# Performance work log

Measured on AMD Instinct MI355X. Metric: run time of the kernel, lower is better.

The kernel has to match this reference:

```python
import jax, jax.numpy as jnp
import numpy as np

B, SQ, SKV, D = 8, 2048, 2048, 1024

def setup_inputs() -> dict:
    key = jax.random.key(0)
    ks = jax.random.split(key, 8)
    s = 1.0 / np.sqrt(D)  # torch Linear default init range
    return {
        "target": jax.random.normal(ks[0], (B, SQ, D), dtype=jnp.float32),
        "non_target": jax.random.normal(ks[1], (B, SKV, D), dtype=jnp.float32),
        "Wq": jax.random.uniform(ks[2], (D, D), jnp.float32, -s, s),
        "bq": jax.random.uniform(ks[3], (D,), jnp.float32, -s, s),
        "Wk": jax.random.uniform(ks[4], (D, D), jnp.float32, -s, s),
        "bk": jax.random.uniform(ks[5], (D,), jnp.float32, -s, s),
        "Wv": jax.random.uniform(ks[6], (D, D), jnp.float32, -s, s),
        "bv": jax.random.uniform(ks[7], (D,), jnp.float32, -s, s),
    }

def reference(target, non_target, Wq, bq, Wk, bk, Wv, bv):
    # Linear projections (torch Linear: x @ W.T + b)
    q = jnp.einsum('bsd,ed->bse', target, Wq) + bq       # [B,SQ,D]
    k = jnp.einsum('bsd,ed->bse', non_target, Wk) + bk   # [B,SKV,D]
    v = jnp.einsum('bsd,ed->bse', non_target, Wv) + bv   # [B,SKV,D]
    # Unscaled attention, exactly as the original module (no 1/sqrt(d))
    scores = jnp.einsum('bqd,bkd->bqk', q, k)            # [B,SQ,SKV]
    weights = jax.nn.softmax(scores, axis=-1)
    return jnp.einsum('bqk,bkd->bqd', weights, v)        # [B,SQ,D]
```

## Files before the change

### kernel.cpp

```cpp
#include <hip/hip_runtime.h>


typedef _Float16 half8 __attribute__((ext_vector_type(8)));
typedef _Float16 half4v __attribute__((ext_vector_type(4)));
typedef float floatx4 __attribute__((ext_vector_type(4)));

__device__ __forceinline__ void async_copy16(const _Float16* g, _Float16* l) {
  __builtin_amdgcn_global_load_lds(
      (const __attribute__((address_space(1))) void*)g,
      (__attribute__((address_space(3))) void*)l,
      16, 0, 0);
}

__global__ __launch_bounds__(256) void cast_all(const float* __restrict__ t,
                                                const float* __restrict__ nt,
                                                const float* __restrict__ wq,
                                                const float* __restrict__ wk,
                                                const float* __restrict__ wv,
                                                _Float16* __restrict__ tgt16,
                                                _Float16* __restrict__ ntg16,
                                                _Float16* __restrict__ wq16,
                                                _Float16* __restrict__ wk16,
                                                _Float16* __restrict__ wv16) {
  const int b = blockIdx.x;
  const float* src;
  _Float16* dst;
  long base;
  if (b < 8192)       { src = t;  dst = tgt16; base = (long)b * 2048; }
  else if (b < 16384) { src = nt; dst = ntg16; base = (long)(b - 8192) * 2048; }
  else if (b < 16896) { src = wq; dst = wq16;  base = (long)(b - 16384) * 2048; }
  else if (b < 17408) { src = wk; dst = wk16;  base = (long)(b - 16896) * 2048; }
  else                { src = wv; dst = wv16;  base = (long)(b - 17408) * 2048; }
  const long i = base + (long)threadIdx.x * 8;
  float4 a = *(const float4*)(src + i);
  float4 c = *(const float4*)(src + i + 4);
  half8 h;
  h[0] = (_Float16)a.x; h[1] = (_Float16)a.y; h[2] = (_Float16)a.z; h[3] = (_Float16)a.w;
  h[4] = (_Float16)c.x; h[5] = (_Float16)c.y; h[6] = (_Float16)c.z; h[7] = (_Float16)c.w;
  *(half8*)(dst + i) = h;
}

template <int OMODE, int SWZ>
__global__ __launch_bounds__(256, 2) void gemm_bt(const _Float16* __restrict__ A,
                                                  const _Float16* __restrict__ B,
                                                  const float* __restrict__ bias,
                                                  const float* __restrict__ biasK,
                                                  const float* __restrict__ biasV,
                                                  void* __restrict__ out,
                                                  int K, int N,
                                                  long sA, long sB, long sO) {
  __shared__ __attribute__((aligned(16))) _Float16 smem[2 * 128 * 64];
  _Float16* As = smem;
  _Float16* Bs = smem + 8192;

  const int tid = threadIdx.x;
  const int lane = tid & 63;
  const int wave = tid >> 6;
  const long bz = blockIdx.z;

  int bx = blockIdx.x, by = blockIdx.y;
  if (SWZ == 1) {
    const int h = bx + 16 * by, g = h & 7, idx = h >> 3;
    bx = (g & 3) * 4 + (idx & 3);
    by = (g >> 2) * 8 + (idx >> 2);
  } else if (SWZ == 2) {
    const int h = bx + 16 * by, g = h & 7, idx = h >> 3;
    bx = (g & 3) * 4 + (idx & 3);
    by = (g >> 2) * 4 + (idx >> 2);
  }

  const long abase = (OMODE == 4 ? (bz ? sA : 0) : bz * sA) + (long)bx * 128 * K;
  const _Float16* Ab = A + abase;
  const _Float16* Bb = B + bz * sB + (long)by * 128 * K;

  const int wm = (wave & 1) * 64;
  const int wn = (wave >> 1) * 64;
  const int frow = lane & 15;
  const int fq = lane >> 4;
  const int fsw = frow & 7;

  floatx4 acc[4][4];
#pragma unroll
  for (int mt = 0; mt < 4; mt++)
#pragma unroll
    for (int nt = 0; nt < 4; nt++)
      acc[mt][nt] = (floatx4){0.f, 0.f, 0.f, 0.f};

  const int sr = tid >> 3;
  const int gl = (tid & 7) ^ (sr & 7);
  const long gOffBase = (long)sr * K + gl * 8;
  const int ldsOff = tid * 8;

  for (int k0 = 0; k0 < K; k0 += 64) {
    __syncthreads();
#pragma unroll
    for (int j = 0; j < 4; j++) {
      async_copy16(Ab + gOffBase + (long)(32 * j) * K + k0, As + ldsOff + j * 2048);
      async_copy16(Bb + gOffBase + (long)(32 * j) * K + k0, Bs + ldsOff + j * 2048);
    }
    __syncthreads();

#pragma unroll
    for (int h = 0; h < 2; h++) {
      half8 af[4], bf[4];
#pragma unroll
      for (int mt = 0; mt < 4; mt++)
        af[mt] = *(const half8*)(As + (wm + mt * 16 + frow) * 64 + ((h * 4 + fq) ^ fsw) * 8);
#pragma unroll
      for (int nt = 0; nt < 4; nt++)
        bf[nt] = *(const half8*)(Bs + (wn + nt * 16 + frow) * 64 + ((h * 4 + fq) ^ fsw) * 8);
#pragma unroll
      for (int mt = 0; mt < 4; mt++)
#pragma unroll
        for (int nt = 0; nt < 4; nt++)
          acc[mt][nt] = __builtin_amdgcn_mfma_f32_16x16x32_f16(af[mt], bf[nt], acc[mt][nt], 0, 0, 0);
    }
  }

  if (OMODE == 2 || OMODE == 3) {
#pragma unroll
    for (int nt = 0; nt < 4; nt++) {
      const int n = by * 128 + wn + nt * 16 + frow;
#pragma unroll
      for (int mt = 0; mt < 4; mt++) {
        const int rbase = bx * 128 + wm + mt * 16 + fq * 4;
#pragma unroll
        for (int i = 0; i < 4; i++) {
          if (OMODE == 2)
            ((float*)out + bz * sO)[(long)(rbase + i) * N + n] = acc[mt][nt][i];
          else
            ((_Float16*)out + bz * sO)[(long)(rbase + i) * N + n] = (_Float16)acc[mt][nt][i];
        }
      }
    }
  } else {
    const float* bp = (bz == 0) ? bias : (bz == 1) ? biasK : biasV;
    if (bz < 2) {
#pragma unroll
      for (int nt = 0; nt < 4; nt++) {
        const int n = by * 128 + wn + nt * 16 + frow;
        const float bvv = bp[n];
        _Float16* o16 = (_Float16*)out + bz * sO;
#pragma unroll
        for (int mt = 0; mt < 4; mt++) {
          const int rbase = bx * 128 + wm + mt * 16 + fq * 4;
#pragma unroll
          for (int i = 0; i < 4; i++)
            o16[(long)(rbase + i) * N + n] = (_Float16)(acc[mt][nt][i] + bvv);
        }
      }
    } else {
      __syncthreads();
#pragma unroll
      for (int nt = 0; nt < 4; nt++) {
        const int c = wn + nt * 16 + frow;
        const float bvv = bp[by * 128 + c];
        const int cx = c & 7;
#pragma unroll
        for (int mt = 0; mt < 4; mt++) {
          const int r0 = wm + mt * 16 + fq * 4;
          half4v hv;
#pragma unroll
          for (int i = 0; i < 4; i++) hv[i] = (_Float16)(acc[mt][nt][i] + bvv);
          *(half4v*)(smem + c * 128 + (((r0 >> 3) ^ cx) << 3) + (r0 & 7)) = hv;
        }
      }
      __syncthreads();
      const long bb = bx >> 4;
      const int sbase = (bx & 15) * 128;
      _Float16* vt = (_Float16*)out + 2 * sO + bb * (2048l * 1024) + sbase;
#pragma unroll
      for (int j = 0; j < 8; j++) {
        const int c = j * 16 + (tid >> 4);
        const int g = tid & 15;
        const int pg = g ^ (c & 7);
        half8 v = *(const half8*)(smem + c * 128 + pg * 8);
        *(half8*)(vt + (long)(by * 128 + c) * 2048 + g * 8) = v;
      }
    }
  }
}

__global__ __launch_bounds__(256) void softmax_rows(const _Float16* __restrict__ S,
                                                    _Float16* __restrict__ P) {
  const long row = blockIdx.x;
  const _Float16* src = S + row * 2048;
  _Float16* dst = P + row * 2048;
  const int tid = threadIdx.x;

  half8 v = ((const half8*)src)[tid];
  float f[8];
#pragma unroll
  for (int i = 0; i < 8; i++) f[i] = (float)v[i];

  float m = fmaxf(fmaxf(fmaxf(f[0], f[1]), fmaxf(f[2], f[3])),
                  fmaxf(fmaxf(f[4], f[5]), fmaxf(f[6], f[7])));
#pragma unroll
  for (int o = 32; o > 0; o >>= 1) m = fmaxf(m, __shfl_xor(m, o, 64));
  __shared__ float redm[4];
  if ((tid & 63) == 0) redm[tid >> 6] = m;
  __syncthreads();
  m = fmaxf(fmaxf(redm[0], redm[1]), fmaxf(redm[2], redm[3]));

  float e[8], s = 0.f;
#pragma unroll
  for (int i = 0; i < 8; i++) { e[i] = __expf(f[i] - m); s += e[i]; }
#pragma unroll
  for (int o = 32; o > 0; o >>= 1) s += __shfl_xor(s, o, 64);
  __shared__ float reds[4];
  if ((tid & 63) == 0) reds[tid >> 6] = s;
  __syncthreads();
  s = (reds[0] + reds[1]) + (reds[2] + reds[3]);
  const float inv = 1.f / s;

  half8 h;
#pragma unroll
  for (int i = 0; i < 8; i++) h[i] = (_Float16)(e[i] * inv);
  ((half8*)dst)[tid] = h;
}

extern "C" void kernel_launch(void* const* d_in, const int* in_sizes, int n_in,
                              void* d_out, int out_size, void* d_ws, size_t ws_size,
                              hipStream_t stream) {
  const float* target = (const float*)d_in[0];
  const float* non_target = (const float*)d_in[1];
  const float* Wq = (const float*)d_in[2];
  const float* bq = (const float*)d_in[3];
  const float* Wk = (const float*)d_in[4];
  const float* bk = (const float*)d_in[5];
  const float* Wv = (const float*)d_in[6];
  const float* bv = (const float*)d_in[7];

  char* ws = (char*)d_ws;
  const size_t MB = 1ull << 20;
  _Float16* tgt16 = (_Float16*)(ws);
  _Float16* ntg16 = (_Float16*)(ws + 32 * MB);
  _Float16* S16 = (_Float16*)(ws);
  _Float16* P16 = (_Float16*)(ws + 64 * MB);
  _Float16* Q16 = (_Float16*)(ws + 128 * MB);
  _Float16* K16 = (_Float16*)(ws + 160 * MB);
  _Float16* Vt16 = (_Float16*)(ws + 192 * MB);
  _Float16* Wq16 = (_Float16*)(ws + 224 * MB);
  _Float16* Wk16 = (_Float16*)(ws + 226 * MB);
  _Float16* Wv16 = (_Float16*)(ws + 228 * MB);

  cast_all<<<17920, 256, 0, stream>>>(target, non_target, Wq, Wk, Wv,
                                      tgt16, ntg16, Wq16, Wk16, Wv16);

  gemm_bt<4, 0><<<dim3(128, 8, 3), 256, 0, stream>>>(
      tgt16, Wq16, bq, bk, bv, Q16, 1024, 1024,
      16777216l, 1048576l, 16777216l);

  gemm_bt<3, 1><<<dim3(16, 16, 8), 256, 0, stream>>>(
      Q16, K16, nullptr, nullptr, nullptr, S16, 1024, 2048,
      2048l * 1024, 2048l * 1024, 2048l * 2048);

  softmax_rows<<<16384, 256, 0, stream>>>(S16, P16);

  gemm_bt<2, 2><<<dim3(16, 8, 8), 256, 0, stream>>>(
      P16, Vt16, nullptr, nullptr, nullptr, (float*)d_out, 2048, 1024,
      2048l * 2048, 1024l * 2048, 2048l * 1024);
}
```

Measured before the change: 453.3 us.

## Fuse K and V projections into one kernel sharing the non_target tile

Splits the combined QKV projection launch into a Q projection and a new gemm_kv kernel that computes K and V together. Each block loads the non_target A tile once and multiplies it against both Wk and Wv tiles, which halves A-tile global loads for the K/V projections. The cost is double the accumulator registers (32 floatx4) and 50% more shared memory per block, which may reduce occupancy or cause spills under launch_bounds(256,2). The kernel also loses the overlap of Q and K/V work within a single launch.

New measurement: 453.0 us. Within noise of the previous version (-0.1%).

```diff
diff --git a/kernel.cpp b/kernel.cpp
--- a/kernel.cpp
+++ b/kernel.cpp
@@ -44,8 +44,6 @@
 __global__ __launch_bounds__(256, 2) void gemm_bt(const _Float16* __restrict__ A,
                                                   const _Float16* __restrict__ B,
                                                   const float* __restrict__ bias,
-                                                  const float* __restrict__ biasK,
-                                                  const float* __restrict__ biasV,
                                                   void* __restrict__ out,
                                                   int K, int N,
                                                   long sA, long sB, long sO) {
@@ -69,8 +67,7 @@
     by = (g >> 2) * 4 + (idx >> 2);
   }
 
-  const long abase = (OMODE == 4 ? (bz ? sA : 0) : bz * sA) + (long)bx * 128 * K;
-  const _Float16* Ab = A + abase;
+  const _Float16* Ab = A + bz * sA + (long)bx * 128 * K;
   const _Float16* Bb = B + bz * sB + (long)by * 128 * K;
 
   const int wm = (wave & 1) * 64;
@@ -134,50 +131,137 @@
       }
     }
   } else {
-    const float* bp = (bz == 0) ? bias : (bz == 1) ? biasK : biasV;
-    if (bz < 2) {
-#pragma unroll
-      for (int nt = 0; nt < 4; nt++) {
-        const int n = by * 128 + wn + nt * 16 + frow;
-        const float bvv = bp[n];
-        _Float16* o16 = (_Float16*)out + bz * sO;
-#pragma unroll
-        for (int mt = 0; mt < 4; mt++) {
-          const int rbase = bx * 128 + wm + mt * 16 + fq * 4;
-#pragma unroll
-          for (int i = 0; i < 4; i++)
-            o16[(long)(rbase + i) * N + n] = (_Float16)(acc[mt][nt][i] + bvv);
-        }
+#pragma unroll
+    for (int nt = 0; nt < 4; nt++) {
+      const int n = by * 128 + wn + nt * 16 + frow;
+      const float bvv = bias[n];
+#pragma unroll
+      for (int mt = 0; mt < 4; mt++) {
+        const int rbase = bx * 128 + wm + mt * 16 + fq * 4;
+#pragma unroll
+        for (int i = 0; i < 4; i++)
+          ((_Float16*)out)[(long)(rbase + i) * N + n] = (_Float16)(acc[mt][nt][i] + bvv);
       }
-    } else {
-      __syncthreads();
-#pragma unroll
-      for (int nt = 0; nt < 4; nt++) {
-        const int c = wn + nt * 16 + frow;
-        const float bvv = bp[by * 128 + c];
-        const int cx = c & 7;
-#pragma unroll
-        for (int mt = 0; mt < 4; mt++) {
-          const int r0 = wm + mt * 16 + fq * 4;
-          half4v hv;
-#pragma unroll
-          for (int i = 0; i < 4; i++) hv[i] = (_Float16)(acc[mt][nt][i] + bvv);
-          *(half4v*)(smem + c * 128 + (((r0 >> 3) ^ cx) << 3) + (r0 & 7)) = hv;
-        }
-      }
-      __syncthreads();
-      const long bb = bx >> 4;
-      const int sbase = (bx & 15) * 128;
-      _Float16* vt = (_Float16*)out + 2 * sO + bb * (2048l * 1024) + sbase;
-#pragma unroll
-      for (int j = 0; j < 8; j++) {
-        const int c = j * 16 + (tid >> 4);
-        const int g = tid & 15;
-        const int pg = g ^ (c & 7);
-        half8 v = *(const half8*)(smem + c * 128 + pg * 8);
-        *(half8*)(vt + (long)(by * 128 + c) * 2048 + g * 8) = v;
-      }
-    }
+    }
+  }
+}
+
+__global__ __launch_bounds__(256, 2) void gemm_kv(const _Float16* __restrict__ A,
+                                                  const _Float16* __restrict__ Bk,
+                                                  const _Float16* __restrict__ Bv,
+                                                  const float* __restrict__ biasK,
+                                                  const float* __restrict__ biasV,
+                                                  _Float16* __restrict__ Kout,
+                                                  _Float16* __restrict__ Vt) {
+  const int K = 1024, N = 1024;
+  __shared__ __attribute__((aligned(16))) _Float16 smem[3 * 128 * 64];
+  _Float16* As = smem;
+  _Float16* BsK = smem + 8192;
+  _Float16* BsV = smem + 16384;
+
+  const int tid = threadIdx.x;
+  const int lane = tid & 63;
+  const int wave = tid >> 6;
+  const int bx = blockIdx.x, by = blockIdx.y;
+
+  const _Float16* Ab = A + (long)bx * 128 * K;
+  const _Float16* BkB = Bk + (long)by * 128 * K;
+  const _Float16* BvB = Bv + (long)by * 128 * K;
+
+  const int wm = (wave & 1) * 64;
+  const int wn = (wave >> 1) * 64;
+  const int frow = lane & 15;
+  const int fq = lane >> 4;
+  const int fsw = frow & 7;
+
+  floatx4 accK[4][4], accV[4][4];
+#pragma unroll
+  for (int mt = 0; mt < 4; mt++)
+#pragma unroll
+    for (int nt = 0; nt < 4; nt++) {
+      accK[mt][nt] = (floatx4){0.f, 0.f, 0.f, 0.f};
+      accV[mt][nt] = (floatx4){0.f, 0.f, 0.f, 0.f};
+    }
+
+  const int sr = tid >> 3;
+  const int gl = (tid & 7) ^ (sr & 7);
+  const long gOffBase = (long)sr * K + gl * 8;
+  const int ldsOff = tid * 8;
+
+  for (int k0 = 0; k0 < K; k0 += 64) {
+    __syncthreads();
+#pragma unroll
+    for (int j = 0; j < 4; j++) {
+      async_copy16(Ab + gOffBase + (long)(32 * j) * K + k0, As + ldsOff + j * 2048);
+      async_copy16(BkB + gOffBase + (long)(32 * j) * K + k0, BsK + ldsOff + j * 2048);
+      async_copy16(BvB + gOffBase + (long)(32 * j) * K + k0, BsV + ldsOff + j * 2048);
+    }
+    __syncthreads();
+
+#pragma unroll
+    for (int h = 0; h < 2; h++) {
+      half8 af[4], bfK[4], bfV[4];
+#pragma unroll
+      for (int mt = 0; mt < 4; mt++)
+        af[mt] = *(const half8*)(As + (wm + mt * 16 + frow) * 64 + ((h * 4 + fq) ^ fsw) * 8);
+#pragma unroll
+      for (int nt = 0; nt < 4; nt++)
+        bfK[nt] = *(const half8*)(BsK + (wn + nt * 16 + frow) * 64 + ((h * 4 + fq) ^ fsw) * 8);
+#pragma unroll
+      for (int mt = 0; mt < 4; mt++)
+#pragma unroll
+        for (int nt = 0; nt < 4; nt++)
+          accK[mt][nt] = __builtin_amdgcn_mfma_f32_16x16x32_f16(af[mt], bfK[nt], accK[mt][nt], 0, 0, 0);
+#pragma unroll
+      for (int nt = 0; nt < 4; nt++)
+        bfV[nt] = *(const half8*)(BsV + (wn + nt * 16 + frow) * 64 + ((h * 4 + fq) ^ fsw) * 8);
+#pragma unroll
+      for (int mt = 0; mt < 4; mt++)
+#pragma unroll
+        for (int nt = 0; nt < 4; nt++)
+          accV[mt][nt] = __builtin_amdgcn_mfma_f32_16x16x32_f16(af[mt], bfV[nt], accV[mt][nt], 0, 0, 0);
+    }
+  }
+
+#pragma unroll
+  for (int nt = 0; nt < 4; nt++) {
+    const int n = by * 128 + wn + nt * 16 + frow;
+    const float bvv = biasK[n];
+#pragma unroll
+    for (int mt = 0; mt < 4; mt++) {
+      const int rbase = bx * 128 + wm + mt * 16 + fq * 4;
+#pragma unroll
+      for (int i = 0; i < 4; i++)
+        Kout[(long)(rbase + i) * N + n] = (_Float16)(accK[mt][nt][i] + bvv);
+    }
+  }
+
+  __syncthreads();
+#pragma unroll
+  for (int nt = 0; nt < 4; nt++) {
+    const int c = wn + nt * 16 + frow;
+    const float bvv = biasV[by * 128 + c];
+    const int cx = c & 7;
+#pragma unroll
+    for (int mt = 0; mt < 4; mt++) {
+      const int r0 = wm + mt * 16 + fq * 4;
+      half4v hv;
+#pragma unroll
+      for (int i = 0; i < 4; i++) hv[i] = (_Float16)(accV[mt][nt][i] + bvv);
+      *(half4v*)(smem + c * 128 + (((r0 >> 3) ^ cx) << 3) + (r0 & 7)) = hv;
+    }
+  }
+  __syncthreads();
+  const long bb = bx >> 4;
+  const int sbase = (bx & 15) * 128;
+  _Float16* vt = Vt + bb * (2048l * 1024) + sbase;
+#pragma unroll
+  for (int j = 0; j < 8; j++) {
+    const int c = j * 16 + (tid >> 4);
+    const int g = tid & 15;
+    const int pg = g ^ (c & 7);
+    half8 v = *(const half8*)(smem + c * 128 + pg * 8);
+    *(half8*)(vt + (long)(by * 128 + c) * 2048 + g * 8) = v;
   }
 }
 
@@ -247,17 +331,18 @@
   cast_all<<<17920, 256, 0, stream>>>(target, non_target, Wq, Wk, Wv,
                                       tgt16, ntg16, Wq16, Wk16, Wv16);
 
-  gemm_bt<4, 0><<<dim3(128, 8, 3), 256, 0, stream>>>(
-      tgt16, Wq16, bq, bk, bv, Q16, 1024, 1024,
-      16777216l, 1048576l, 16777216l);
+  gemm_bt<0, 0><<<dim3(128, 8, 1), 256, 0, stream>>>(
+      tgt16, Wq16, bq, Q16, 1024, 1024, 0, 0, 0);
+
+  gemm_kv<<<dim3(128, 8), 256, 0, stream>>>(ntg16, Wk16, Wv16, bk, bv, K16, Vt16);
 
   gemm_bt<3, 1><<<dim3(16, 16, 8), 256, 0, stream>>>(
-      Q16, K16, nullptr, nullptr, nullptr, S16, 1024, 2048,
+      Q16, K16, nullptr, S16, 1024, 2048,
       2048l * 1024, 2048l * 1024, 2048l * 2048);
 
   softmax_rows<<<16384, 256, 0, stream>>>(S16, P16);
 
   gemm_bt<2, 2><<<dim3(16, 8, 8), 256, 0, stream>>>(
-      P16, Vt16, nullptr, nullptr, nullptr, (float*)d_out, 2048, 1024,
+      P16, Vt16, nullptr, (float*)d_out, 2048, 1024,
       2048l * 2048, 1024l * 2048, 2048l * 1024);
 }
```
